# Performance work log

Hardware: AMD Instinct MI355X
Metric: run time of the kernel (lower is better)

The kernel has to match this reference:

```python
import jax, jax.numpy as jnp
import numpy as np

N_NODES = 100000
N_EDGES = 1600000
D_IN = 128
D_HID = 128
N_CLS = 2


def gcn_conv(x, edge_index, W, b):
    """PyG GCNConv: add self-loops, symmetric normalization, linear, scatter-add, bias."""
    n = x.shape[0]
    loop = jnp.arange(n, dtype=edge_index.dtype)
    src = jnp.concatenate([edge_index[0], loop])  # [E+N]
    dst = jnp.concatenate([edge_index[1], loop])
    # degree computed on destination (col) after adding self-loops
    deg = jax.ops.segment_sum(jnp.ones_like(dst, dtype=x.dtype), dst, num_segments=n)
    dinv = jnp.where(deg > 0, jax.lax.rsqrt(deg), 0.0)
    norm = dinv[src] * dinv[dst]  # [E+N]
    h = x @ W  # [N, out]
    msg = h[src] * norm[:, None]  # [E+N, out]
    out = jax.ops.segment_sum(msg, dst, num_segments=n)
    return out + b


def setup_inputs() -> dict:
    key = jax.random.key(0)
    k1, k2, k3, k4 = jax.random.split(key, 4)
    x = jax.random.normal(k1, (N_NODES, D_IN), dtype=jnp.float32)
    edge_index = jax.random.randint(k2, (2, N_EDGES), 0, N_NODES, dtype=jnp.int64)
    W1 = jax.random.normal(k3, (D_IN, D_HID), dtype=jnp.float32) * (1.0 / np.sqrt(D_IN))
    b1 = jnp.zeros((D_HID,), dtype=jnp.float32)
    W2 = jax.random.normal(k4, (D_HID, N_CLS), dtype=jnp.float32) * (1.0 / np.sqrt(D_HID))
    b2 = jnp.zeros((N_CLS,), dtype=jnp.float32)
    return {"x": x, "edge_index": edge_index, "W1": W1, "b1": b1, "W2": W2, "b2": b2}


def reference(x, edge_index, W1, b1, W2, b2):
    h = gcn_conv(x, edge_index, W1, b1)
    h = jax.nn.relu(h)
    # training=False -> dropout skipped
    out = gcn_conv(h, edge_index, W2, b2)
    return out
```

## Files before the change

### kernel.cpp

```cpp
#include <hip/hip_runtime.h>
#include <hip/hip_fp16.h>
#include <cstdint>
#include <cstddef>

#define NN 100000
#define NE 1600000
#define D 128
#define NBK 782
#define NBLK_P 200
#define EPB 8000
#define CAP 3072

typedef _Float16 half8 __attribute__((ext_vector_type(8)));
typedef _Float16 half4v __attribute__((ext_vector_type(4)));
typedef float f32x4 __attribute__((ext_vector_type(4)));


__launch_bounds__(256)
__global__ void pscat_k(const int* __restrict__ ei, unsigned* __restrict__ gcnt,
                        unsigned* __restrict__ part,
                        const float* __restrict__ W, _Float16* __restrict__ Wt) {
    __shared__ unsigned hist[NBK];
    __shared__ unsigned run[NBK];
    int tid = threadIdx.x, b = blockIdx.x;
    for (int k = tid; k < NBK; k += 256) hist[k] = 0u;
    __syncthreads();
    int e0 = b * EPB;
    for (int i = tid * 4; i < EPB; i += 1024) {
        int4 d4 = *(const int4*)(ei + NE + e0 + i);
        atomicAdd(&hist[d4.x >> 7], 1u);
        atomicAdd(&hist[d4.y >> 7], 1u);
        atomicAdd(&hist[d4.z >> 7], 1u);
        atomicAdd(&hist[d4.w >> 7], 1u);
    }
    __syncthreads();
    for (int k = tid; k < NBK; k += 256) {
        unsigned c = hist[k];
        run[k] = c ? atomicAdd(&gcnt[k * 16], c) : 0u;
    }
    if (b < 64) {
        int idx = b * 256 + tid;
        int n = idx >> 7, kk = idx & 127;
        Wt[idx] = (_Float16)W[kk * 128 + n];
    }
    __syncthreads();
    for (int i = tid * 4; i < EPB; i += 1024) {
        int4 s4 = *(const int4*)(ei + e0 + i);
        int4 d4 = *(const int4*)(ei + NE + e0 + i);
        unsigned k, slot;
        k = (unsigned)(d4.x >> 7); slot = atomicAdd(&run[k], 1u);
        if (slot < CAP) part[(size_t)k * CAP + slot] = (unsigned)s4.x | ((unsigned)(d4.x & 127) << 20);
        k = (unsigned)(d4.y >> 7); slot = atomicAdd(&run[k], 1u);
        if (slot < CAP) part[(size_t)k * CAP + slot] = (unsigned)s4.y | ((unsigned)(d4.y & 127) << 20);
        k = (unsigned)(d4.z >> 7); slot = atomicAdd(&run[k], 1u);
        if (slot < CAP) part[(size_t)k * CAP + slot] = (unsigned)s4.z | ((unsigned)(d4.z & 127) << 20);
        k = (unsigned)(d4.w >> 7); slot = atomicAdd(&run[k], 1u);
        if (slot < CAP) part[(size_t)k * CAP + slot] = (unsigned)s4.w | ((unsigned)(d4.w & 127) << 20);
    }
}

__launch_bounds__(256)
__global__ void p4g_k(const unsigned* __restrict__ part, const unsigned* __restrict__ gcnt,
                      const float* __restrict__ x, const _Float16* __restrict__ Wt,
                      unsigned* __restrict__ rp, unsigned* __restrict__ re,
                      float* __restrict__ dinv, unsigned* __restrict__ col,
                      _Float16* __restrict__ h) {
    __shared__ __align__(16) _Float16 wt[128 * 136];
    __shared__ __align__(16) _Float16 xs[128 * 72];
    __shared__ float dinvs[128];
    unsigned* cc  = (unsigned*)xs;
    unsigned* pp  = cc + 128;
    unsigned* run = pp + 128;
    int tid = threadIdx.x, k = blockIdx.x;
    int n0 = k << 7;
    int nodes = (NN - n0 < 128) ? (NN - n0) : 128;
    int w = tid >> 6, lane = tid & 63;
    int m = lane & 15, q4 = lane >> 4;

#pragma unroll
    for (int q = 0; q < 8; q++) {
        int idx = q * 256 + tid;
        int n = idx >> 4, k8 = (idx & 15) * 8;
        *(half8*)(&wt[n * 136 + k8]) = *(const half8*)(Wt + n * 128 + k8);
    }

    unsigned cnt = gcnt[k * 16];
    if (cnt > CAP) cnt = CAP;
    unsigned e0c = (unsigned)k * CAP;
    const unsigned* pk = part + (size_t)k * CAP;

    if (tid < 128) cc[tid] = 0u;
    __syncthreads();
    for (unsigned t = tid; t < cnt; t += 256)
        atomicAdd(&cc[(pk[t] >> 20) & 127], 1u);
    __syncthreads();

    unsigned myc = (tid < 128) ? cc[tid] : 0u;
    if (tid < 128) pp[tid] = myc;
    __syncthreads();
    for (int off = 1; off < 128; off <<= 1) {
        unsigned u = 0;
        if (tid < 128 && tid >= off) u = pp[tid - off];
        __syncthreads();
        if (tid < 128) pp[tid] += u;
        __syncthreads();
    }
    if (tid < 128) {
        unsigned excl = pp[tid] - myc;
        run[tid] = excl;
        float dv = rsqrtf((float)(myc + 1u));
        dinvs[tid] = dv;
        if (tid < nodes) {
            rp[n0 + tid] = e0c + excl;
            re[n0 + tid] = e0c + excl + myc;
            dinv[n0 + tid] = dv;
        }
    }
    __syncthreads();

    for (unsigned t = tid; t < cnt; t += 256) {
        unsigned v = pk[t];
        unsigned dlo = (v >> 20) & 127;
        unsigned pos = e0c + atomicAdd(&run[dlo], 1u);
        col[pos] = v & 0xFFFFFu;
    }
    __syncthreads();

    f32x4 acc[2][8];
#pragma unroll
    for (int rt = 0; rt < 2; rt++)
#pragma unroll
        for (int nt = 0; nt < 8; nt++) acc[rt][nt] = (f32x4){0.f, 0.f, 0.f, 0.f};

    for (int ks = 0; ks <= 64; ks += 64) {
        if (ks) __syncthreads();
#pragma unroll
        for (int q = 0; q < 8; q++) {
            int idx = q * 256 + tid;
            int row = idx >> 4;
            int c4 = (idx & 15) * 4;
            int gr = n0 + row;
            float4 v = (gr < NN) ? *(const float4*)(x + (size_t)gr * 128 + ks + c4)
                                 : make_float4(0, 0, 0, 0);
            half4v hv = { (_Float16)v.x, (_Float16)v.y, (_Float16)v.z, (_Float16)v.w };
            *(half4v*)(&xs[row * 72 + c4]) = hv;
        }
        __syncthreads();

#pragma unroll
        for (int kc = 0; kc < 2; kc++) {
            half8 a0 = *(const half8*)(&xs[(w * 32 + m) * 72 + kc * 32 + q4 * 8]);
            half8 a1 = *(const half8*)(&xs[(w * 32 + 16 + m) * 72 + kc * 32 + q4 * 8]);
#pragma unroll
            for (int nt = 0; nt < 8; nt++) {
                half8 bf = *(const half8*)(&wt[(nt * 16 + m) * 136 + ks + kc * 32 + q4 * 8]);
                acc[0][nt] = __builtin_amdgcn_mfma_f32_16x16x32_f16(a0, bf, acc[0][nt], 0, 0, 0);
                acc[1][nt] = __builtin_amdgcn_mfma_f32_16x16x32_f16(a1, bf, acc[1][nt], 0, 0, 0);
            }
        }
    }

    float dv[2][4];
#pragma unroll
    for (int rt = 0; rt < 2; rt++)
#pragma unroll
        for (int r = 0; r < 4; r++)
            dv[rt][r] = dinvs[w * 32 + rt * 16 + q4 * 4 + r];
    __syncthreads();
#pragma unroll
    for (int rt = 0; rt < 2; rt++)
#pragma unroll
        for (int nt = 0; nt < 8; nt++)
#pragma unroll
            for (int r = 0; r < 4; r++)
                wt[(w * 32 + rt * 16 + q4 * 4 + r) * 136 + nt * 16 + m] =
                    (_Float16)(acc[rt][nt][r] * dv[rt][r]);
    __syncthreads();
#pragma unroll
    for (int q = 0; q < 8; q++) {
        int idx = q * 256 + tid;
        int row = idx >> 4;
        int c8 = (idx & 15) * 8;
        int gr = n0 + row;
        if (gr < NN)
            *(half8*)(h + (size_t)gr * 128 + c8) = *(const half8*)(&wt[row * 136 + c8]);
    }
}

__launch_bounds__(256)
__global__ void agg1_k(const _Float16* __restrict__ h, const unsigned* __restrict__ rp,
                       const unsigned* __restrict__ re, const unsigned* __restrict__ col,
                       const float* __restrict__ dinv, const float* __restrict__ b1,
                       const float* __restrict__ W2, float* __restrict__ z) {
    int i = (blockIdx.x * 256 + threadIdx.x) >> 6;
    int lane = threadIdx.x & 63;
    if (i >= NN) return;
    unsigned si = __builtin_amdgcn_readfirstlane((unsigned)i);

    const __half2* hb = (const __half2*)h;
    unsigned p0 = __builtin_amdgcn_readfirstlane(rp[si]);
    unsigned p1 = __builtin_amdgcn_readfirstlane(re[si]);
    int deg = (int)(p1 - p0);

    unsigned cv = col[p0 + (unsigned)lane];

    int degc = deg > 64 ? 64 : deg;
    int R = (degc + 15) >> 4;
    float2 sv = __half22float2(hb[(size_t)si * 64u + lane]);
    float f = (float)(1 + degc - 16 * R);
    float ax = f * sv.x, ay = f * sv.y;

#define ROUND16(r)                                                           \
    {                                                                        \
        float2 vv[16];                                                       \
        _Pragma("unroll")                                                    \
        for (int t = 0; t < 16; t++) {                                       \
            int k = (r) * 16 + t;                                            \
            unsigned s = (k < degc) ? __builtin_amdgcn_readlane(cv, k) : si; \
            vv[t] = __half22float2(hb[(size_t)s * 64u + lane]);              \
        }                                                                    \
        ax += ((vv[0].x + vv[1].x) + (vv[2].x + vv[3].x))                    \
            + ((vv[4].x + vv[5].x) + (vv[6].x + vv[7].x))                    \
            + ((vv[8].x + vv[9].x) + (vv[10].x + vv[11].x))                  \
            + ((vv[12].x + vv[13].x) + (vv[14].x + vv[15].x));               \
        ay += ((vv[0].y + vv[1].y) + (vv[2].y + vv[3].y))                    \
            + ((vv[4].y + vv[5].y) + (vv[6].y + vv[7].y))                    \
            + ((vv[8].y + vv[9].y) + (vv[10].y + vv[11].y))                  \
            + ((vv[12].y + vv[13].y) + (vv[14].y + vv[15].y));               \
    }

    if (degc > 0)  ROUND16(0)
    if (degc > 16) ROUND16(1)
    if (degc > 32) ROUND16(2)
    if (degc > 48) ROUND16(3)
#undef ROUND16

    for (unsigned e = p0 + 64; e < p1; ++e) {
        unsigned s_ = __builtin_amdgcn_readfirstlane(col[e]);
        float2 v = __half22float2(hb[(size_t)s_ * 64u + lane]);
        ax += v.x;
        ay += v.y;
    }

    float di = dinv[si];
    ax *= di;
    ay *= di;

    float2 bv = ((const float2*)b1)[lane];
    float h0 = fmaxf(ax + bv.x, 0.f);
    float h1 = fmaxf(ay + bv.y, 0.f);

    float4 w = ((const float4*)W2)[lane];
    float pz0 = fmaf(h0, w.x, h1 * w.z);
    float pz1 = fmaf(h0, w.y, h1 * w.w);
#pragma unroll
    for (int off = 32; off > 0; off >>= 1) {
        pz0 += __shfl_down(pz0, off);
        pz1 += __shfl_down(pz1, off);
    }
    if (lane == 0) {
        float2* zp = (float2*)(z + (size_t)si * 2);
        *zp = make_float2(pz0 * di, pz1 * di);
    }
}

__launch_bounds__(256)
__global__ void agg2_k(const float* __restrict__ z, const unsigned* __restrict__ rp,
                       const unsigned* __restrict__ re, const unsigned* __restrict__ col,
                       const float* __restrict__ dinv, const float* __restrict__ b2,
                       float* __restrict__ out) {
    int i = (blockIdx.x * 256 + threadIdx.x) >> 4;
    int sl = threadIdx.x & 15;
    if (i >= NN) return;

    unsigned p0 = rp[i], p1 = re[i];
    float a0 = 0.f, a1 = 0.f;
    for (unsigned e = p0 + sl; e < p1; e += 16) {
        unsigned s = col[e];
        float2 v = ((const float2*)z)[s];
        a0 += v.x;
        a1 += v.y;
    }
#pragma unroll
    for (int off = 8; off > 0; off >>= 1) {
        a0 += __shfl_down(a0, off, 16);
        a1 += __shfl_down(a1, off, 16);
    }
    if (sl == 0) {
        float di = dinv[i];
        float2 zi = ((const float2*)z)[i];
        out[(size_t)i * 2]     = (a0 + zi.x) * di + b2[0];
        out[(size_t)i * 2 + 1] = (a1 + zi.y) * di + b2[1];
    }
}

extern "C" void kernel_launch(void* const* d_in, const int* in_sizes, int n_in,
                              void* d_out, int out_size, void* d_ws, size_t ws_size,
                              hipStream_t stream) {
    const float* x  = (const float*)d_in[0];
    const int*   ei = (const int*)d_in[1];
    const float* W1 = (const float*)d_in[2];
    const float* b1 = (const float*)d_in[3];
    const float* W2 = (const float*)d_in[4];
    const float* b2 = (const float*)d_in[5];
    float* out = (float*)d_out;

    char* ws = (char*)d_ws;
    unsigned* part = (unsigned*)(ws);
    unsigned* gcnt = (unsigned*)(ws + 9609216);
    float*    z    = (float*)(ws + 25600000);
    float*    dinv = (float*)(ws + 26400000);
    unsigned* rp   = (unsigned*)(ws + 26800000);
    unsigned* re   = (unsigned*)(ws + 27200000);
    unsigned* col  = (unsigned*)(ws + 27600000);
    _Float16* Wt   = (_Float16*)(ws + 37300000);
    _Float16* h    = (_Float16*)(ws + 40000000);

    hipMemsetAsync(gcnt, 0, 782 * 16 * sizeof(unsigned), stream);
    pscat_k<<<NBLK_P, 256, 0, stream>>>(ei, gcnt, part, W1, Wt);
    p4g_k<<<NBK, 256, 0, stream>>>(part, gcnt, x, Wt, rp, re, dinv, col, h);
    agg1_k<<<(NN * 64 + 255) / 256, 256, 0, stream>>>(h, rp, re, col, dinv, b1, W2, z);
    agg2_k<<<(NN * 16 + 255) / 256, 256, 0, stream>>>(z, rp, re, col, dinv, b2, out);
}
```

Before: 219.6 us.

## Replace bucketed CSR build with fixed-slot per-node adjacency via global atomics

The two-pass bucket partition and in-block prefix-sum CSR construction is replaced by a single scatter kernel. It atomically increments a per-destination counter and writes each source into a fixed 64-slot row for that node. The GEMM kernel then only computes dinv from the counters, and both aggregation kernels index columns directly by node*64. The aim is to remove the intermediate partition buffer, the extra read/write pass and the shared-memory scans. In exchange it relies on many contended global atomics, uses a padded column array, and silently drops any edges past 64 per node, since the overflow loop was removed.

New measurement: 317.9 us. +44.8%, slower.

```diff
diff --git a/kernel.cpp b/kernel.cpp
--- a/kernel.cpp
+++ b/kernel.cpp
@@ -7,9 +7,7 @@
 #define NE 1600000
 #define D 128
 #define NBK 782
-#define NBLK_P 200
-#define EPB 8000
-#define CAP 3072
+#define SLOTS 64
 
 typedef _Float16 half8 __attribute__((ext_vector_type(8)));
 typedef _Float16 half4v __attribute__((ext_vector_type(4)));
@@ -17,63 +15,39 @@
 
 
 __launch_bounds__(256)
-__global__ void pscat_k(const int* __restrict__ ei, unsigned* __restrict__ gcnt,
-                        unsigned* __restrict__ part,
-                        const float* __restrict__ W, _Float16* __restrict__ Wt) {
-    __shared__ unsigned hist[NBK];
-    __shared__ unsigned run[NBK];
-    int tid = threadIdx.x, b = blockIdx.x;
-    for (int k = tid; k < NBK; k += 256) hist[k] = 0u;
-    __syncthreads();
-    int e0 = b * EPB;
-    for (int i = tid * 4; i < EPB; i += 1024) {
-        int4 d4 = *(const int4*)(ei + NE + e0 + i);
-        atomicAdd(&hist[d4.x >> 7], 1u);
-        atomicAdd(&hist[d4.y >> 7], 1u);
-        atomicAdd(&hist[d4.z >> 7], 1u);
-        atomicAdd(&hist[d4.w >> 7], 1u);
-    }
-    __syncthreads();
-    for (int k = tid; k < NBK; k += 256) {
-        unsigned c = hist[k];
-        run[k] = c ? atomicAdd(&gcnt[k * 16], c) : 0u;
-    }
+__global__ void scat_k(const int* __restrict__ ei, unsigned* __restrict__ cnt,
+                       unsigned* __restrict__ col,
+                       const float* __restrict__ W, _Float16* __restrict__ Wt) {
+    int b = blockIdx.x, tid = threadIdx.x;
     if (b < 64) {
         int idx = b * 256 + tid;
         int n = idx >> 7, kk = idx & 127;
         Wt[idx] = (_Float16)W[kk * 128 + n];
     }
-    __syncthreads();
-    for (int i = tid * 4; i < EPB; i += 1024) {
-        int4 s4 = *(const int4*)(ei + e0 + i);
-        int4 d4 = *(const int4*)(ei + NE + e0 + i);
-        unsigned k, slot;
-        k = (unsigned)(d4.x >> 7); slot = atomicAdd(&run[k], 1u);
-        if (slot < CAP) part[(size_t)k * CAP + slot] = (unsigned)s4.x | ((unsigned)(d4.x & 127) << 20);
-        k = (unsigned)(d4.y >> 7); slot = atomicAdd(&run[k], 1u);
-        if (slot < CAP) part[(size_t)k * CAP + slot] = (unsigned)s4.y | ((unsigned)(d4.y & 127) << 20);
-        k = (unsigned)(d4.z >> 7); slot = atomicAdd(&run[k], 1u);
-        if (slot < CAP) part[(size_t)k * CAP + slot] = (unsigned)s4.z | ((unsigned)(d4.z & 127) << 20);
-        k = (unsigned)(d4.w >> 7); slot = atomicAdd(&run[k], 1u);
-        if (slot < CAP) part[(size_t)k * CAP + slot] = (unsigned)s4.w | ((unsigned)(d4.w & 127) << 20);
-    }
-}
-
-__launch_bounds__(256)
-__global__ void p4g_k(const unsigned* __restrict__ part, const unsigned* __restrict__ gcnt,
-                      const float* __restrict__ x, const _Float16* __restrict__ Wt,
-                      unsigned* __restrict__ rp, unsigned* __restrict__ re,
-                      float* __restrict__ dinv, unsigned* __restrict__ col,
-                      _Float16* __restrict__ h) {
+    int i4 = (b * 256 + tid) * 4;
+    if (i4 >= NE) return;
+    int4 s4 = *(const int4*)(ei + i4);
+    int4 d4 = *(const int4*)(ei + NE + i4);
+    unsigned k, pos;
+    k = (unsigned)d4.x; pos = atomicAdd(&cnt[k], 1u);
+    if (pos < SLOTS) col[(size_t)k * SLOTS + pos] = (unsigned)s4.x;
+    k = (unsigned)d4.y; pos = atomicAdd(&cnt[k], 1u);
+    if (pos < SLOTS) col[(size_t)k * SLOTS + pos] = (unsigned)s4.y;
+    k = (unsigned)d4.z; pos = atomicAdd(&cnt[k], 1u);
+    if (pos < SLOTS) col[(size_t)k * SLOTS + pos] = (unsigned)s4.z;
+    k = (unsigned)d4.w; pos = atomicAdd(&cnt[k], 1u);
+    if (pos < SLOTS) col[(size_t)k * SLOTS + pos] = (unsigned)s4.w;
+}
+
+__launch_bounds__(256)
+__global__ void gemm1_k(const float* __restrict__ x, const _Float16* __restrict__ Wt,
+                        const unsigned* __restrict__ cnt, float* __restrict__ dinv,
+                        _Float16* __restrict__ h) {
     __shared__ __align__(16) _Float16 wt[128 * 136];
     __shared__ __align__(16) _Float16 xs[128 * 72];
     __shared__ float dinvs[128];
-    unsigned* cc  = (unsigned*)xs;
-    unsigned* pp  = cc + 128;
-    unsigned* run = pp + 128;
-    int tid = threadIdx.x, k = blockIdx.x;
-    int n0 = k << 7;
-    int nodes = (NN - n0 < 128) ? (NN - n0) : 128;
+    int tid = threadIdx.x;
+    int rb = blockIdx.x * 128;
     int w = tid >> 6, lane = tid & 63;
     int m = lane & 15, q4 = lane >> 4;
 
@@ -83,48 +57,13 @@
         int n = idx >> 4, k8 = (idx & 15) * 8;
         *(half8*)(&wt[n * 136 + k8]) = *(const half8*)(Wt + n * 128 + k8);
     }
-
-    unsigned cnt = gcnt[k * 16];
-    if (cnt > CAP) cnt = CAP;
-    unsigned e0c = (unsigned)k * CAP;
-    const unsigned* pk = part + (size_t)k * CAP;
-
-    if (tid < 128) cc[tid] = 0u;
-    __syncthreads();
-    for (unsigned t = tid; t < cnt; t += 256)
-        atomicAdd(&cc[(pk[t] >> 20) & 127], 1u);
-    __syncthreads();
-
-    unsigned myc = (tid < 128) ? cc[tid] : 0u;
-    if (tid < 128) pp[tid] = myc;
-    __syncthreads();
-    for (int off = 1; off < 128; off <<= 1) {
-        unsigned u = 0;
-        if (tid < 128 && tid >= off) u = pp[tid - off];
-        __syncthreads();
-        if (tid < 128) pp[tid] += u;
-        __syncthreads();
-    }
     if (tid < 128) {
-        unsigned excl = pp[tid] - myc;
-        run[tid] = excl;
-        float dv = rsqrtf((float)(myc + 1u));
+        int gr = rb + tid;
+        unsigned c = (gr < NN) ? cnt[gr] : 0u;
+        float dv = rsqrtf((float)(c + 1u));
         dinvs[tid] = dv;
-        if (tid < nodes) {
-            rp[n0 + tid] = e0c + excl;
-            re[n0 + tid] = e0c + excl + myc;
-            dinv[n0 + tid] = dv;
-        }
-    }
-    __syncthreads();
-
-    for (unsigned t = tid; t < cnt; t += 256) {
-        unsigned v = pk[t];
-        unsigned dlo = (v >> 20) & 127;
-        unsigned pos = e0c + atomicAdd(&run[dlo], 1u);
-        col[pos] = v & 0xFFFFFu;
-    }
-    __syncthreads();
+        if (gr < NN) dinv[gr] = dv;
+    }
 
     f32x4 acc[2][8];
 #pragma unroll
@@ -139,7 +78,7 @@
             int idx = q * 256 + tid;
             int row = idx >> 4;
             int c4 = (idx & 15) * 4;
-            int gr = n0 + row;
+            int gr = rb + row;
             float4 v = (gr < NN) ? *(const float4*)(x + (size_t)gr * 128 + ks + c4)
                                  : make_float4(0, 0, 0, 0);
             half4v hv = { (_Float16)v.x, (_Float16)v.y, (_Float16)v.z, (_Float16)v.w };
@@ -181,28 +120,26 @@
         int idx = q * 256 + tid;
         int row = idx >> 4;
         int c8 = (idx & 15) * 8;
-        int gr = n0 + row;
+        int gr = rb + row;
         if (gr < NN)
             *(half8*)(h + (size_t)gr * 128 + c8) = *(const half8*)(&wt[row * 136 + c8]);
     }
 }
 
 __launch_bounds__(256)
-__global__ void agg1_k(const _Float16* __restrict__ h, const unsigned* __restrict__ rp,
-                       const unsigned* __restrict__ re, const unsigned* __restrict__ col,
-                       const float* __restrict__ dinv, const float* __restrict__ b1,
-                       const float* __restrict__ W2, float* __restrict__ z) {
+__global__ void agg1_k(const _Float16* __restrict__ h, const unsigned* __restrict__ cnt,
+                       const unsigned* __restrict__ col, const float* __restrict__ dinv,
+                       const float* __restrict__ b1, const float* __restrict__ W2,
+                       float* __restrict__ z) {
     int i = (blockIdx.x * 256 + threadIdx.x) >> 6;
     int lane = threadIdx.x & 63;
     if (i >= NN) return;
     unsigned si = __builtin_amdgcn_readfirstlane((unsigned)i);
 
     const __half2* hb = (const __half2*)h;
-    unsigned p0 = __builtin_amdgcn_readfirstlane(rp[si]);
-    unsigned p1 = __builtin_amdgcn_readfirstlane(re[si]);
-    int deg = (int)(p1 - p0);
-
-    unsigned cv = col[p0 + (unsigned)lane];
+    int deg = (int)__builtin_amdgcn_readfirstlane(cnt[si]);
+
+    unsigned cv = col[(size_t)si * SLOTS + (unsigned)lane];
 
     int degc = deg > 64 ? 64 : deg;
     int R = (degc + 15) >> 4;
@@ -235,13 +172,6 @@
     if (degc > 48) ROUND16(3)
 #undef ROUND16
 
-    for (unsigned e = p0 + 64; e < p1; ++e) {
-        unsigned s_ = __builtin_amdgcn_readfirstlane(col[e]);
-        float2 v = __half22float2(hb[(size_t)s_ * 64u + lane]);
-        ax += v.x;
-        ay += v.y;
-    }
-
     float di = dinv[si];
     ax *= di;
     ay *= di;
@@ -265,15 +195,16 @@
 }
 
 __launch_bounds__(256)
-__global__ void agg2_k(const float* __restrict__ z, const unsigned* __restrict__ rp,
-                       const unsigned* __restrict__ re, const unsigned* __restrict__ col,
-                       const float* __restrict__ dinv, const float* __restrict__ b2,
-                       float* __restrict__ out) {
+__global__ void agg2_k(const float* __restrict__ z, const unsigned* __restrict__ cnt,
+                       const unsigned* __restrict__ col, const float* __restrict__ dinv,
+                       const float* __restrict__ b2, float* __restrict__ out) {
     int i = (blockIdx.x * 256 + threadIdx.x) >> 4;
     int sl = threadIdx.x & 15;
     if (i >= NN) return;
 
-    unsigned p0 = rp[i], p1 = re[i];
+    unsigned deg = cnt[i];
+    if (deg > SLOTS) deg = SLOTS;
+    unsigned p0 = (unsigned)i * SLOTS, p1 = p0 + deg;
     float a0 = 0.f, a1 = 0.f;
     for (unsigned e = p0 + sl; e < p1; e += 16) {
         unsigned s = col[e];
@@ -306,19 +237,16 @@
     float* out = (float*)d_out;
 
     char* ws = (char*)d_ws;
-    unsigned* part = (unsigned*)(ws);
-    unsigned* gcnt = (unsigned*)(ws + 9609216);
-    float*    z    = (float*)(ws + 25600000);
-    float*    dinv = (float*)(ws + 26400000);
-    unsigned* rp   = (unsigned*)(ws + 26800000);
-    unsigned* re   = (unsigned*)(ws + 27200000);
-    unsigned* col  = (unsigned*)(ws + 27600000);
-    _Float16* Wt   = (_Float16*)(ws + 37300000);
-    _Float16* h    = (_Float16*)(ws + 40000000);
-
-    hipMemsetAsync(gcnt, 0, 782 * 16 * sizeof(unsigned), stream);
-    pscat_k<<<NBLK_P, 256, 0, stream>>>(ei, gcnt, part, W1, Wt);
-    p4g_k<<<NBK, 256, 0, stream>>>(part, gcnt, x, Wt, rp, re, dinv, col, h);
-    agg1_k<<<(NN * 64 + 255) / 256, 256, 0, stream>>>(h, rp, re, col, dinv, b1, W2, z);
-    agg2_k<<<(NN * 16 + 255) / 256, 256, 0, stream>>>(z, rp, re, col, dinv, b2, out);
-}
+    unsigned* cnt  = (unsigned*)(ws);
+    float*    dinv = (float*)(ws + 400000);
+    float*    z    = (float*)(ws + 800000);
+    _Float16* Wt   = (_Float16*)(ws + 1600000);
+    unsigned* col  = (unsigned*)(ws + 1638400);
+    _Float16* h    = (_Float16*)(ws + 27238400);
+
+    hipMemsetAsync(cnt, 0, NN * sizeof(unsigned), stream);
+    scat_k<<<(NE / 4 + 255) / 256, 256, 0, stream>>>(ei, cnt, col, W1, Wt);
+    gemm1_k<<<NBK, 256, 0, stream>>>(x, Wt, cnt, dinv, h);
+    agg1_k<<<(NN * 64 + 255) / 256, 256, 0, stream>>>(h, cnt, col, dinv, b1, W2, z);
+    agg2_k<<<(NN * 16 + 255) / 256, 256, 0, stream>>>(z, cnt, col, dinv, b2, out);
+}
```

## Load GEMM A operands directly from global, use wave-shuffle scan in p4g_k

Applied to the files above, without the earlier changes.

Removes the xs shared-memory staging of x. Each lane now loads its own fp32 row fragments from global, converts them to half and feeds them straight into the MFMA, which drops the staging barriers and frees LDS. The 128-entry prefix scan over shared memory with repeated syncthreads becomes a single-wave shuffle scan. Launch bounds now request 4 blocks per SM. In exchange the global loads of x are less coalesced (strided per-row 32-byte reads), and register pressure rises under the tighter occupancy bound.

Result: faster. 212.7 us, median of 2 (-3.1%).

```diff
diff --git a/kernel.cpp b/kernel.cpp
--- a/kernel.cpp
+++ b/kernel.cpp
@@ -12,7 +12,6 @@
 #define CAP 3072
 
 typedef _Float16 half8 __attribute__((ext_vector_type(8)));
-typedef _Float16 half4v __attribute__((ext_vector_type(4)));
 typedef float f32x4 __attribute__((ext_vector_type(4)));
 
 
@@ -59,21 +58,18 @@
     }
 }
 
-__launch_bounds__(256)
+__launch_bounds__(256, 4)
 __global__ void p4g_k(const unsigned* __restrict__ part, const unsigned* __restrict__ gcnt,
                       const float* __restrict__ x, const _Float16* __restrict__ Wt,
                       unsigned* __restrict__ rp, unsigned* __restrict__ re,
                       float* __restrict__ dinv, unsigned* __restrict__ col,
                       _Float16* __restrict__ h) {
     __shared__ __align__(16) _Float16 wt[128 * 136];
-    __shared__ __align__(16) _Float16 xs[128 * 72];
+    __shared__ unsigned cc[128];
+    __shared__ unsigned run[128];
     __shared__ float dinvs[128];
-    unsigned* cc  = (unsigned*)xs;
-    unsigned* pp  = cc + 128;
-    unsigned* run = pp + 128;
     int tid = threadIdx.x, k = blockIdx.x;
     int n0 = k << 7;
-    int nodes = (NN - n0 < 128) ? (NN - n0) : 128;
     int w = tid >> 6, lane = tid & 63;
     int m = lane & 15, q4 = lane >> 4;
 
@@ -95,26 +91,30 @@
         atomicAdd(&cc[(pk[t] >> 20) & 127], 1u);
     __syncthreads();
 
-    unsigned myc = (tid < 128) ? cc[tid] : 0u;
-    if (tid < 128) pp[tid] = myc;
-    __syncthreads();
-    for (int off = 1; off < 128; off <<= 1) {
-        unsigned u = 0;
-        if (tid < 128 && tid >= off) u = pp[tid - off];
-        __syncthreads();
-        if (tid < 128) pp[tid] += u;
-        __syncthreads();
-    }
-    if (tid < 128) {
-        unsigned excl = pp[tid] - myc;
-        run[tid] = excl;
-        float dv = rsqrtf((float)(myc + 1u));
-        dinvs[tid] = dv;
-        if (tid < nodes) {
-            rp[n0 + tid] = e0c + excl;
-            re[n0 + tid] = e0c + excl + myc;
-            dinv[n0 + tid] = dv;
+    if (tid < 64) {
+        unsigned c0 = cc[tid], c1 = cc[64 + tid];
+        unsigned v0 = c0, v1 = c1;
+#pragma unroll
+        for (int off = 1; off < 64; off <<= 1) {
+            unsigned u = __shfl_up(v0, off);
+            if (tid >= off) v0 += u;
         }
+#pragma unroll
+        for (int off = 1; off < 64; off <<= 1) {
+            unsigned u = __shfl_up(v1, off);
+            if (tid >= off) v1 += u;
+        }
+        v1 += __shfl(v0, 63);
+        unsigned ex0 = v0 - c0, ex1 = v1 - c1;
+        run[tid] = ex0;
+        run[64 + tid] = ex1;
+        float dv0 = rsqrtf((float)(c0 + 1u));
+        float dv1 = rsqrtf((float)(c1 + 1u));
+        dinvs[tid] = dv0;
+        dinvs[64 + tid] = dv1;
+        int g0 = n0 + tid, g1 = n0 + 64 + tid;
+        if (g0 < NN) { rp[g0] = e0c + ex0; re[g0] = e0c + ex0 + c0; dinv[g0] = dv0; }
+        if (g1 < NN) { rp[g1] = e0c + ex1; re[g1] = e0c + ex1 + c1; dinv[g1] = dv1; }
     }
     __syncthreads();
 
@@ -124,7 +124,12 @@
         unsigned pos = e0c + atomicAdd(&run[dlo], 1u);
         col[pos] = v & 0xFFFFFu;
     }
-    __syncthreads();
+
+    int r0 = n0 + w * 32 + m;
+    int r1 = r0 + 16;
+    bool ok0 = r0 < NN, ok1 = r1 < NN;
+    const float* xr0 = x + (size_t)r0 * 128 + q4 * 8;
+    const float* xr1 = x + (size_t)r1 * 128 + q4 * 8;
 
     f32x4 acc[2][8];
 #pragma unroll
@@ -132,31 +137,21 @@
 #pragma unroll
         for (int nt = 0; nt < 8; nt++) acc[rt][nt] = (f32x4){0.f, 0.f, 0.f, 0.f};
 
-    for (int ks = 0; ks <= 64; ks += 64) {
-        if (ks) __syncthreads();
-#pragma unroll
-        for (int q = 0; q < 8; q++) {
-            int idx = q * 256 + tid;
-            int row = idx >> 4;
-            int c4 = (idx & 15) * 4;
-            int gr = n0 + row;
-            float4 v = (gr < NN) ? *(const float4*)(x + (size_t)gr * 128 + ks + c4)
-                                 : make_float4(0, 0, 0, 0);
-            half4v hv = { (_Float16)v.x, (_Float16)v.y, (_Float16)v.z, (_Float16)v.w };
-            *(half4v*)(&xs[row * 72 + c4]) = hv;
-        }
-        __syncthreads();
-
-#pragma unroll
-        for (int kc = 0; kc < 2; kc++) {
-            half8 a0 = *(const half8*)(&xs[(w * 32 + m) * 72 + kc * 32 + q4 * 8]);
-            half8 a1 = *(const half8*)(&xs[(w * 32 + 16 + m) * 72 + kc * 32 + q4 * 8]);
-#pragma unroll
-            for (int nt = 0; nt < 8; nt++) {
-                half8 bf = *(const half8*)(&wt[(nt * 16 + m) * 136 + ks + kc * 32 + q4 * 8]);
-                acc[0][nt] = __builtin_amdgcn_mfma_f32_16x16x32_f16(a0, bf, acc[0][nt], 0, 0, 0);
-                acc[1][nt] = __builtin_amdgcn_mfma_f32_16x16x32_f16(a1, bf, acc[1][nt], 0, 0, 0);
-            }
+#pragma unroll
+    for (int ks = 0; ks < 128; ks += 32) {
+        float4 f00 = ok0 ? *(const float4*)(xr0 + ks)     : make_float4(0, 0, 0, 0);
+        float4 f01 = ok0 ? *(const float4*)(xr0 + ks + 4) : make_float4(0, 0, 0, 0);
+        float4 f10 = ok1 ? *(const float4*)(xr1 + ks)     : make_float4(0, 0, 0, 0);
+        float4 f11 = ok1 ? *(const float4*)(xr1 + ks + 4) : make_float4(0, 0, 0, 0);
+        half8 a0 = { (_Float16)f00.x, (_Float16)f00.y, (_Float16)f00.z, (_Float16)f00.w,
+                     (_Float16)f01.x, (_Float16)f01.y, (_Float16)f01.z, (_Float16)f01.w };
+        half8 a1 = { (_Float16)f10.x, (_Float16)f10.y, (_Float16)f10.z, (_Float16)f10.w,
+                     (_Float16)f11.x, (_Float16)f11.y, (_Float16)f11.z, (_Float16)f11.w };
+#pragma unroll
+        for (int nt = 0; nt < 8; nt++) {
+            half8 bf = *(const half8*)(&wt[(nt * 16 + m) * 136 + ks + q4 * 8]);
+            acc[0][nt] = __builtin_amdgcn_mfma_f32_16x16x32_f16(a0, bf, acc[0][nt], 0, 0, 0);
+            acc[1][nt] = __builtin_amdgcn_mfma_f32_16x16x32_f16(a1, bf, acc[1][nt], 0, 0, 0);
         }
     }
 
```
